# Kernel tuning notes

Measured on AMD Instinct MI355X. Metric: run time of the kernel, lower is better.

## Reference

```python
import jax, jax.numpy as jnp
import numpy as np

L, N, E, H = 2048, 2, 1024, 16
D = E // H  # head dim = 64


def setup_inputs() -> dict:
    key = jax.random.key(0)
    k1, k2, k3, k4, k5 = jax.random.split(key, 5)
    s = 1.0 / np.sqrt(E)
    return {
        "x": jax.random.normal(k1, (L, N, E), dtype=jnp.float32),
        "in_proj_weight": jax.random.normal(k2, (3 * E, E), dtype=jnp.float32) * s,
        "in_proj_bias": jax.random.normal(k3, (3 * E,), dtype=jnp.float32) * 0.01,
        "out_proj_weight": jax.random.normal(k4, (E, E), dtype=jnp.float32) * s,
        "out_proj_bias": jax.random.normal(k5, (E,), dtype=jnp.float32) * 0.01,
    }


def reference(x, in_proj_weight, in_proj_bias, out_proj_weight, out_proj_bias):
    # packed qkv in-projection: (L, N, 3E)
    qkv = jnp.einsum("lne,fe->lnf", x, in_proj_weight) + in_proj_bias
    q, k, v = jnp.split(qkv, 3, axis=-1)

    def heads(t):  # (L, N, E) -> (N, H, L, D)
        return t.reshape(L, N, H, D).transpose(1, 2, 0, 3)

    q, k, v = heads(q), heads(k), heads(v)
    scale = 1.0 / jnp.sqrt(jnp.asarray(D, dtype=q.dtype))
    scores = jnp.einsum("nhld,nhmd->nhlm", q * scale, k)  # (N, H, L, L)
    attn = jax.nn.softmax(scores, axis=-1)
    out = jnp.einsum("nhlm,nhmd->nhld", attn, v)  # (N, H, L, D)
    out = out.transpose(2, 0, 1, 3).reshape(L, N, E)
    return jnp.einsum("lne,fe->lnf", out, out_proj_weight) + out_proj_bias
```

## Files before the change

kernel.cpp:

```cpp
#include <hip/hip_runtime.h>

typedef __attribute__((ext_vector_type(8))) short bf16x8;
typedef __attribute__((ext_vector_type(4))) float f32x4;
typedef __attribute__((ext_vector_type(16))) float f32x16;
typedef __attribute__((ext_vector_type(8))) unsigned short ushort8;
typedef __attribute__((ext_vector_type(4))) unsigned short ushort4_t;
typedef __attribute__((ext_vector_type(4))) unsigned uint4_t;

#define LSEQ 2048
#define NB 2
#define EMB 1024
#define NHEAD 16
#define HD 64

__device__ __forceinline__ unsigned short f2bf(float f) {
  unsigned u = __builtin_bit_cast(unsigned, f);
  u += 0x7fffu + ((u >> 16) & 1u);
  return (unsigned short)(u >> 16);
}
__device__ __forceinline__ float bf2f(unsigned short s) {
  return __builtin_bit_cast(float, ((unsigned)s) << 16);
}

__device__ __forceinline__ void gll16(const void* g, void* l) {
  __builtin_amdgcn_global_load_lds((const __attribute__((address_space(1))) unsigned*)g,
                                   (__attribute__((address_space(3))) unsigned*)l, 16, 0, 0);
}

__global__ __launch_bounds__(256) void cvt_all(const float* __restrict__ x,
                                               const float* __restrict__ wq,
                                               const float* __restrict__ wo,
                                               unsigned short* __restrict__ xb,
                                               unsigned short* __restrict__ wqb,
                                               unsigned short* __restrict__ wob) {
  int i = blockIdx.x * 256 + threadIdx.x;
  const float* src;
  unsigned short* dst;
  int off;
  if (i < 1048576) { src = x;  dst = xb;  off = i; }
  else if (i < 1835008) { src = wq; dst = wqb; off = i - 1048576; }
  else { src = wo; dst = wob; off = i - 1835008; }
  float4 v = ((const float4*)src)[off];
  ushort4_t o;
  o.x = f2bf(v.x); o.y = f2bf(v.y); o.z = f2bf(v.z); o.w = f2bf(v.w);
  ((ushort4_t*)dst)[off] = o;
}

template <bool OUT_BF16>
__global__ __launch_bounds__(256, 2) void gemm_bf16_nt(
    const unsigned short* __restrict__ A, const unsigned short* __restrict__ B,
    const float* __restrict__ bias, void* __restrict__ Cout, int M, int Ncol, int K) {
  __shared__ unsigned short Asm[2][128 * 64];
  __shared__ unsigned short Bsm[2][128 * 64];
  const int tid = threadIdx.x;
  const int wave = tid >> 6, lane = tid & 63;
  const int wr = (wave >> 1) * 64, wc = (wave & 1) * 64;
  const int lr = lane & 15, lg = lane >> 4;
  const int bm = blockIdx.x * 128, bn = blockIdx.y * 128;

  f32x4 acc[4][4];
#pragma unroll
  for (int i = 0; i < 4; ++i)
#pragma unroll
    for (int j = 0; j < 4; ++j) acc[i][j] = (f32x4){0.f, 0.f, 0.f, 0.f};

  auto stage = [&](int buf, int kt) {
#pragma unroll
    for (int c = 0; c < 4; ++c) {
      int idx = (c * 4 + wave) * 64 + lane;
      int row = idx >> 3, ch = (idx & 7) * 8;
      gll16(A + (size_t)(bm + row) * K + kt * 64 + ch, &Asm[buf][(c * 4 + wave) * 512]);
      gll16(B + (size_t)(bn + row) * K + kt * 64 + ch, &Bsm[buf][(c * 4 + wave) * 512]);
    }
  };

  const int nk = K >> 6;
  stage(0, 0);
  __syncthreads();
  int cur = 0;

  for (int kt = 0; kt < nk; ++kt) {
    if (kt < nk - 1) stage(cur ^ 1, kt + 1);
#pragma unroll
    for (int ks = 0; ks < 2; ++ks) {
      bf16x8 af[4], bfr[4];
#pragma unroll
      for (int i = 0; i < 4; ++i)
        af[i] = *(const bf16x8*)&Asm[cur][(wr + i * 16 + lr) * 64 + ks * 32 + lg * 8];
#pragma unroll
      for (int j = 0; j < 4; ++j)
        bfr[j] = *(const bf16x8*)&Bsm[cur][(wc + j * 16 + lr) * 64 + ks * 32 + lg * 8];
      __builtin_amdgcn_s_setprio(1);
#pragma unroll
      for (int i = 0; i < 4; ++i)
#pragma unroll
        for (int j = 0; j < 4; ++j)
          acc[i][j] = __builtin_amdgcn_mfma_f32_16x16x32_bf16(af[i], bfr[j], acc[i][j], 0, 0, 0);
      __builtin_amdgcn_s_setprio(0);
    }
    __syncthreads();
    cur ^= 1;
  }
#pragma unroll
  for (int i = 0; i < 4; ++i) {
#pragma unroll
    for (int j = 0; j < 4; ++j) {
      int col = bn + wc + j * 16 + lr;
      float bv = bias[col];
#pragma unroll
      for (int r = 0; r < 4; ++r) {
        int row = bm + wr + i * 16 + lg * 4 + r;
        float v = acc[i][j][r] + bv;
        if constexpr (OUT_BF16)
          ((unsigned short*)Cout)[(size_t)row * Ncol + col] = f2bf(v);
        else
          ((float*)Cout)[(size_t)row * Ncol + col] = v;
      }
    }
  }
}

__global__ __launch_bounds__(256) void transpose_v(const unsigned short* __restrict__ qkv,
                                                   unsigned short* __restrict__ vt) {
  __shared__ unsigned short t[64][72];
  const int nh = blockIdx.y, n = nh >> 4, h = nh & 15;
  const int lt = blockIdx.x * 64;
  const int tid = threadIdx.x;
#pragma unroll
  for (int it = 0; it < 2; ++it) {
    int idx = it * 256 + tid;
    int l = idx >> 3, ch = (idx & 7) * 8;
    ushort8 v = *(const ushort8*)(qkv + (size_t)((lt + l) * NB + n) * 3072 + 2 * EMB + h * HD + ch);
    *(ushort8*)&t[l][ch] = v;
  }
  __syncthreads();
  int d = tid >> 2, lc = (tid & 3) * 16;
  unsigned short tmp[16];
#pragma unroll
  for (int i = 0; i < 16; ++i) tmp[i] = t[lc + i][d];
#pragma unroll
  for (int i = 0; i < 2; ++i)
    *(ushort8*)(vt + (size_t)(nh * HD + d) * LSEQ + lt + lc + i * 8) = *(const ushort8*)&tmp[i * 8];
}

__global__ __launch_bounds__(256, 4) void flash_attn(const unsigned short* __restrict__ qkv,
                                                     const unsigned short* __restrict__ vt,
                                                     float* __restrict__ Op,
                                                     float* __restrict__ Lp) {
  __shared__ unsigned short Ksm[2][64 * 64];
  __shared__ unsigned short Vsm[2][64 * 64];
  const int tid = threadIdx.x, wave = tid >> 6, lane = tid & 63;
  const int l31 = lane & 31, lh = lane >> 5;
  const int flat = blockIdx.x;
  const int fb = (flat & 7) * 128 + (flat >> 3);
  const int nh = fb >> 5, rem = fb & 31;
  const int qt = rem >> 1, half = rem & 1;
  const int n = nh >> 4, hh = nh & 15;
  const int q = qt * 128 + wave * 32 + l31;
  const int key0 = half * (LSEQ / 2);

  const int sch = ((lane & 7) ^ ((lane >> 3) & 7)) * 8;
  const unsigned short* Kbase = qkv + (size_t)n * 3072 + EMB + hh * HD + sch;
  const unsigned short* Vbase = vt + (size_t)nh * HD * LSEQ + sch;

  bf16x8 qf[4];
  {
    const unsigned short* qb = qkv + ((size_t)q * NB + n) * 3072 + hh * HD + lh * 8;
#pragma unroll
    for (int t = 0; t < 4; ++t) {
      bf16x8 tv = *(const bf16x8*)(qb + t * 16);
#pragma unroll
      for (int e = 0; e < 8; ++e)
        tv[e] = (short)f2bf(bf2f((unsigned short)tv[e]) * 0.18033688f);
      qf[t] = tv;
    }
  }

  auto stage = [&](int buf, int kt) {
#pragma unroll
    for (int c = 0; c < 2; ++c) {
      int row = ((c * 4 + wave) * 64 + lane) >> 3;
      gll16(Kbase + (size_t)(key0 + kt * 64 + row) * (NB * 3072), &Ksm[buf][(c * 4 + wave) * 512]);
      gll16(Vbase + (size_t)row * LSEQ + key0 + kt * 64, &Vsm[buf][(c * 4 + wave) * 512]);
    }
  };

  float lsum = 0.f;
  f32x16 o0, o1;
#pragma unroll
  for (int r = 0; r < 16; ++r) { o0[r] = 0.f; o1[r] = 0.f; }

  stage(0, 0);
  __syncthreads();
  int cur = 0;
  const int swz = l31 & 7;
  const int NT = (LSEQ / 2) / 64;

  for (int kt = 0; kt < NT; ++kt) {
    if (kt < NT - 1) stage(cur ^ 1, kt + 1);

    f32x16 s0, s1;
#pragma unroll
    for (int r = 0; r < 16; ++r) { s0[r] = 0.f; s1[r] = 0.f; }
    __builtin_amdgcn_s_setprio(1);
#pragma unroll
    for (int t = 0; t < 4; ++t) {
      int ch = ((t * 2 + lh) ^ swz) * 8;
      bf16x8 k0 = *(const bf16x8*)&Ksm[cur][l31 * 64 + ch];
      bf16x8 k1 = *(const bf16x8*)&Ksm[cur][(32 + l31) * 64 + ch];
      s0 = __builtin_amdgcn_mfma_f32_32x32x16_bf16(k0, qf[t], s0, 0, 0, 0);
      s1 = __builtin_amdgcn_mfma_f32_32x32x16_bf16(k1, qf[t], s1, 0, 0, 0);
    }
    __builtin_amdgcn_s_setprio(0);

    float ps0 = 0.f, ps1 = 0.f, ps2 = 0.f, ps3 = 0.f;
#pragma unroll
    for (int r = 0; r < 16; r += 4) {
      float a0 = exp2f(s0[r]),     b0 = exp2f(s1[r]);
      float a1 = exp2f(s0[r + 1]), b1 = exp2f(s1[r + 1]);
      float a2 = exp2f(s0[r + 2]), b2 = exp2f(s1[r + 2]);
      float a3 = exp2f(s0[r + 3]), b3 = exp2f(s1[r + 3]);
      s0[r] = a0; s0[r + 1] = a1; s0[r + 2] = a2; s0[r + 3] = a3;
      s1[r] = b0; s1[r + 1] = b1; s1[r + 2] = b2; s1[r + 3] = b3;
      ps0 += a0 + b0; ps1 += a1 + b1; ps2 += a2 + b2; ps3 += a3 + b3;
    }
    lsum += (ps0 + ps1) + (ps2 + ps3);

    bf16x8 pf[4];
#pragma unroll
    for (int g = 0; g < 4; ++g) {
      const int b = (g & 1) * 8;
      float a0 = (g < 2) ? s0[b + 0] : s1[b + 0];
      float a1 = (g < 2) ? s0[b + 1] : s1[b + 1];
      float a2 = (g < 2) ? s0[b + 2] : s1[b + 2];
      float a3 = (g < 2) ? s0[b + 3] : s1[b + 3];
      float a4 = (g < 2) ? s0[b + 4] : s1[b + 4];
      float a5 = (g < 2) ? s0[b + 5] : s1[b + 5];
      float a6 = (g < 2) ? s0[b + 6] : s1[b + 6];
      float a7 = (g < 2) ? s0[b + 7] : s1[b + 7];
      unsigned w0, w1, w2, w3;
      asm("v_cvt_pk_bf16_f32 %0, %1, %2" : "=v"(w0) : "v"(a0), "v"(a1));
      asm("v_cvt_pk_bf16_f32 %0, %1, %2" : "=v"(w1) : "v"(a2), "v"(a3));
      asm("v_cvt_pk_bf16_f32 %0, %1, %2" : "=v"(w2) : "v"(a4), "v"(a5));
      asm("v_cvt_pk_bf16_f32 %0, %1, %2" : "=v"(w3) : "v"(a6), "v"(a7));
      asm("v_permlane32_swap_b32 %0, %1" : "+v"(w0), "+v"(w2));
      asm("v_permlane32_swap_b32 %0, %1" : "+v"(w1), "+v"(w3));
      pf[g] = __builtin_bit_cast(bf16x8, (uint4_t){w0, w1, w2, w3});
    }

    __builtin_amdgcn_s_setprio(1);
#pragma unroll
    for (int u = 0; u < 4; ++u) {
      int ch = ((u * 2 + lh) ^ swz) * 8;
      bf16x8 a0 = *(const bf16x8*)&Vsm[cur][l31 * 64 + ch];
      bf16x8 a1 = *(const bf16x8*)&Vsm[cur][(32 + l31) * 64 + ch];
      o0 = __builtin_amdgcn_mfma_f32_32x32x16_bf16(a0, pf[u], o0, 0, 0, 0);
      o1 = __builtin_amdgcn_mfma_f32_32x32x16_bf16(a1, pf[u], o1, 0, 0, 0);
    }
    __builtin_amdgcn_s_setprio(0);

    __syncthreads();
    cur ^= 1;
  }

  float* op = Op + (size_t)half * (4096 * 1024) + ((size_t)q * NB + n) * EMB + hh * HD;
#pragma unroll
  for (int g = 0; g < 4; ++g) {
    float4 pk0, pk1;
    pk0.x = o0[g * 4 + 0]; pk0.y = o0[g * 4 + 1]; pk0.z = o0[g * 4 + 2]; pk0.w = o0[g * 4 + 3];
    pk1.x = o1[g * 4 + 0]; pk1.y = o1[g * 4 + 1]; pk1.z = o1[g * 4 + 2]; pk1.w = o1[g * 4 + 3];
    *(float4*)(op + g * 8 + lh * 4) = pk0;
    *(float4*)(op + 32 + g * 8 + lh * 4) = pk1;
  }
  lsum += __shfl_xor(lsum, 32);
  if (lh == 0)
    Lp[(size_t)half * 65536 + ((size_t)q * NB + n) * NHEAD + hh] = lsum;
}

__global__ __launch_bounds__(256) void combine_o(const float* __restrict__ Op,
                                                 const float* __restrict__ Lp,
                                                 unsigned short* __restrict__ ob) {
  int i = blockIdx.x * 256 + threadIdx.x;
  float4 a = ((const float4*)Op)[i];
  float4 b = ((const float4*)(Op + 4096 * 1024))[i];
  int e = i << 2;
  int qn = e >> 10, h = (e >> 6) & 15;
  float l = Lp[qn * NHEAD + h] + Lp[65536 + qn * NHEAD + h];
  float inv = 1.0f / l;
  ushort4_t o;
  o.x = f2bf((a.x + b.x) * inv);
  o.y = f2bf((a.y + b.y) * inv);
  o.z = f2bf((a.z + b.z) * inv);
  o.w = f2bf((a.w + b.w) * inv);
  ((ushort4_t*)ob)[i] = o;
}

extern "C" void kernel_launch(void* const* d_in, const int* in_sizes, int n_in,
                              void* d_out, int out_size, void* d_ws, size_t ws_size,
                              hipStream_t stream) {
  const float* x = (const float*)d_in[0];
  const float* wqkv = (const float*)d_in[1];
  const float* bqkv = (const float*)d_in[2];
  const float* wout = (const float*)d_in[3];
  const float* bout = (const float*)d_in[4];

  char* ws = (char*)d_ws;
  unsigned short* xb    = (unsigned short*)(ws);
  unsigned short* wqkvb = (unsigned short*)(ws + 8388608);
  unsigned short* woutb = (unsigned short*)(ws + 14680064);
  unsigned short* qkvb  = (unsigned short*)(ws + 16777216);
  unsigned short* vtb   = (unsigned short*)(ws + 41943040);
  unsigned short* obuf  = (unsigned short*)(ws + 50331648);
  float*          Op    = (float*)(ws + 58720256);
  float*          Lp    = (float*)(ws + 92274688);

  cvt_all<<<8192, 256, 0, stream>>>(x, wqkv, wout, xb, wqkvb, woutb);

  dim3 g1(32, 24);
  gemm_bf16_nt<true><<<g1, 256, 0, stream>>>(xb, wqkvb, bqkv, qkvb, 4096, 3072, 1024);

  dim3 gt(32, 32);
  transpose_v<<<gt, 256, 0, stream>>>(qkvb, vtb);

  flash_attn<<<1024, 256, 0, stream>>>(qkvb, vtb, Op, Lp);
  combine_o<<<4096, 256, 0, stream>>>(Op, Lp, obuf);

  dim3 g3(32, 8);
  gemm_bf16_nt<false><<<g3, 256, 0, stream>>>(obuf, woutb, bout, d_out, 4096, 1024, 1024);
}
```

Before: 219.0 us.

## Single-buffer GEMM LDS for higher occupancy and drop score accumulator zeroing

The GEMM kernel moves from double-buffered to single-buffered LDS tiles and raises the launch-bounds occupancy hint from 2 to 3 blocks per CU. The aim is to get more resident waves to hide load latency, at the cost of losing the explicit prefetch overlap: each k-step now loads, syncs, computes and syncs again. Separately, the attention kernel no longer zeroes the score accumulators every tile. Its first MFMA instead takes a constant zero vector as input, which removes per-iteration register moves.

```diff
diff --git a/kernel.cpp b/kernel.cpp
--- a/kernel.cpp
+++ b/kernel.cpp
@@ -47,11 +47,11 @@
 }
 
 template <bool OUT_BF16>
-__global__ __launch_bounds__(256, 2) void gemm_bf16_nt(
+__global__ __launch_bounds__(256, 3) void gemm_bf16_nt(
     const unsigned short* __restrict__ A, const unsigned short* __restrict__ B,
     const float* __restrict__ bias, void* __restrict__ Cout, int M, int Ncol, int K) {
-  __shared__ unsigned short Asm[2][128 * 64];
-  __shared__ unsigned short Bsm[2][128 * 64];
+  __shared__ unsigned short Asm[128 * 64];
+  __shared__ unsigned short Bsm[128 * 64];
   const int tid = threadIdx.x;
   const int wave = tid >> 6, lane = tid & 63;
   const int wr = (wave >> 1) * 64, wc = (wave & 1) * 64;
@@ -64,32 +64,24 @@
 #pragma unroll
     for (int j = 0; j < 4; ++j) acc[i][j] = (f32x4){0.f, 0.f, 0.f, 0.f};
 
-  auto stage = [&](int buf, int kt) {
+  for (int kt = 0; kt < K; kt += 64) {
 #pragma unroll
     for (int c = 0; c < 4; ++c) {
       int idx = (c * 4 + wave) * 64 + lane;
       int row = idx >> 3, ch = (idx & 7) * 8;
-      gll16(A + (size_t)(bm + row) * K + kt * 64 + ch, &Asm[buf][(c * 4 + wave) * 512]);
-      gll16(B + (size_t)(bn + row) * K + kt * 64 + ch, &Bsm[buf][(c * 4 + wave) * 512]);
-    }
-  };
-
-  const int nk = K >> 6;
-  stage(0, 0);
-  __syncthreads();
-  int cur = 0;
-
-  for (int kt = 0; kt < nk; ++kt) {
-    if (kt < nk - 1) stage(cur ^ 1, kt + 1);
+      gll16(A + (size_t)(bm + row) * K + kt + ch, &Asm[(c * 4 + wave) * 512]);
+      gll16(B + (size_t)(bn + row) * K + kt + ch, &Bsm[(c * 4 + wave) * 512]);
+    }
+    __syncthreads();
 #pragma unroll
     for (int ks = 0; ks < 2; ++ks) {
       bf16x8 af[4], bfr[4];
 #pragma unroll
       for (int i = 0; i < 4; ++i)
-        af[i] = *(const bf16x8*)&Asm[cur][(wr + i * 16 + lr) * 64 + ks * 32 + lg * 8];
+        af[i] = *(const bf16x8*)&Asm[(wr + i * 16 + lr) * 64 + ks * 32 + lg * 8];
 #pragma unroll
       for (int j = 0; j < 4; ++j)
-        bfr[j] = *(const bf16x8*)&Bsm[cur][(wc + j * 16 + lr) * 64 + ks * 32 + lg * 8];
+        bfr[j] = *(const bf16x8*)&Bsm[(wc + j * 16 + lr) * 64 + ks * 32 + lg * 8];
       __builtin_amdgcn_s_setprio(1);
 #pragma unroll
       for (int i = 0; i < 4; ++i)
@@ -99,7 +91,6 @@
       __builtin_amdgcn_s_setprio(0);
     }
     __syncthreads();
-    cur ^= 1;
   }
 #pragma unroll
   for (int i = 0; i < 4; ++i) {
@@ -186,9 +177,9 @@
   };
 
   float lsum = 0.f;
-  f32x16 o0, o1;
-#pragma unroll
-  for (int r = 0; r < 16; ++r) { o0[r] = 0.f; o1[r] = 0.f; }
+  f32x16 o0, o1, zv;
+#pragma unroll
+  for (int r = 0; r < 16; ++r) { o0[r] = 0.f; o1[r] = 0.f; zv[r] = 0.f; }
 
   stage(0, 0);
   __syncthreads();
@@ -200,11 +191,16 @@
     if (kt < NT - 1) stage(cur ^ 1, kt + 1);
 
     f32x16 s0, s1;
-#pragma unroll
-    for (int r = 0; r < 16; ++r) { s0[r] = 0.f; s1[r] = 0.f; }
     __builtin_amdgcn_s_setprio(1);
-#pragma unroll
-    for (int t = 0; t < 4; ++t) {
+    {
+      int ch = (lh ^ swz) * 8;
+      bf16x8 k0 = *(const bf16x8*)&Ksm[cur][l31 * 64 + ch];
+      bf16x8 k1 = *(const bf16x8*)&Ksm[cur][(32 + l31) * 64 + ch];
+      s0 = __builtin_amdgcn_mfma_f32_32x32x16_bf16(k0, qf[0], zv, 0, 0, 0);
+      s1 = __builtin_amdgcn_mfma_f32_32x32x16_bf16(k1, qf[0], zv, 0, 0, 0);
+    }
+#pragma unroll
+    for (int t = 1; t < 4; ++t) {
       int ch = ((t * 2 + lh) ^ swz) * 8;
       bf16x8 k0 = *(const bf16x8*)&Ksm[cur][l31 * 64 + ch];
       bf16x8 k1 = *(const bf16x8*)&Ksm[cur][(32 + l31) * 64 + ch];
```

Measured after the change: 210.4 us. 3.9% less time.
